# Optimization experiments

Hardware: AMD Instinct MI355X
Metric: run time of the kernel (lower is better)

Reference implementation:

```python
import math
import jax, jax.numpy as jnp
import numpy as np

N, CH3, T = 64, 192, 2048

def setup_inputs() -> dict:
    key = jax.random.key(0)
    qkv = jax.random.normal(key, (N, CH3, T), dtype=jnp.float32)
    return {"qkv": qkv}

def reference(qkv):
    ch = qkv.shape[1] // 3
    q, k, v = jnp.split(qkv, 3, axis=1)  # each [b, c, t]
    scale = 1.0 / math.sqrt(math.sqrt(ch))
    # [b, t, s] score matrix (faithful to the naive implementation)
    weight = jnp.einsum('bct,bcs->bts', q * scale, k * scale)
    weight = jax.nn.softmax(weight.astype(jnp.float32), axis=-1).astype(weight.dtype)
    return jnp.einsum('bts,bcs->bct', weight, v)
```

## Files before the change

kernel.cpp:

```cpp
#include <hip/hip_runtime.h>
#include <math.h>


#define B_     64
#define CH_    64
#define T_     2048
#define TQ     128
#define SB     64
#define NIT    (T_ / SB)
#define TILE_E 4096

typedef __attribute__((ext_vector_type(8))) short short8;
typedef __attribute__((ext_vector_type(4))) float f32x4;
typedef __attribute__((ext_vector_type(16))) float f32x16;
typedef __attribute__((ext_vector_type(4))) unsigned short us4;
typedef __attribute__((ext_vector_type(8))) unsigned short us8;

static __device__ __forceinline__ unsigned short f2bf(float f) {
    union { float f; unsigned u; } v; v.f = f;
    unsigned r = v.u + 0x7FFFu + ((v.u >> 16) & 1u);
    return (unsigned short)(r >> 16);
}

static __device__ __forceinline__ short8 ld_contig(const unsigned short* p) {
    return *(const short8*)p;
}

static __device__ __forceinline__ short8 ld_strided(const unsigned short* p, int stride) {
    short8 r;
#pragma unroll
    for (int j = 0; j < 8; ++j) r[j] = (short)p[j * stride];
    return r;
}

static __device__ __forceinline__ void gl_lds16(const unsigned short* g, unsigned short* l) {
    __builtin_amdgcn_global_load_lds(
        (const __attribute__((address_space(1))) unsigned int*)g,
        (__attribute__((address_space(3))) unsigned int*)l, 16, 0, 0);
}

static __device__ __forceinline__ float vexp2(float x) {
#if __has_builtin(__builtin_amdgcn_exp2f)
    return __builtin_amdgcn_exp2f(x);
#else
    float r;
    asm("v_exp_f32 %0, %1\n\ts_nop 1" : "=v"(r) : "v"(x));
    return r;
#endif
}

static __device__ __forceinline__ unsigned cvtpk(float lo, float hi) {
    unsigned r;
    asm("v_cvt_pk_bf16_f32 %0, %1, %2" : "=v"(r) : "v"(lo), "v"(hi));
    return r;
}

static __device__ __forceinline__ void pl32(unsigned& a, unsigned& b) {
    asm("v_permlane32_swap_b32 %0, %1" : "+v"(a), "+v"(b));
}

static __device__ __forceinline__ void pl_swap(unsigned& a, unsigned& b) {
    asm("v_permlane32_swap_b32 %0, %1" : "+v"(a), "+v"(b));
    asm("v_permlane16_swap_b32 %0, %1" : "+v"(a), "+v"(b));
}

__global__ __launch_bounds__(256) void qkv_prep(const float* __restrict__ qkv,
                                                unsigned short* __restrict__ Ktg,
                                                unsigned short* __restrict__ Vbg)
{
    __shared__ float Tl[64][65];
    const int tid = threadIdx.x;
    const int b   = blockIdx.x >> 5;
    const int st  = blockIdx.x & 31;
    const int s0  = st * 64;
    const float* Kp = qkv + (size_t)b * (3 * CH_ * T_) + (size_t)CH_ * T_;
    const float* Vp = Kp + (size_t)CH_ * T_;
    const size_t tbase = (size_t)(b * 32 + st) * TILE_E;

    {
        const int c = tid & 63, fq = tid >> 6;
#pragma unroll
        for (int k = 0; k < 4; ++k) {
            const int tl = 16 * fq + 4 * k;
            const float4 v = *(const float4*)(Kp + (size_t)c * T_ + s0 + tl);
            Tl[c][tl] = v.x; Tl[c][tl + 1] = v.y; Tl[c][tl + 2] = v.z; Tl[c][tl + 3] = v.w;
        }
    }

    {
        const int R = tid >> 2;
        const int m = tid & 3;
        const float* vin = Vp + (size_t)R * T_ + s0 + 16 * m;
        const float4 a0 = *(const float4*)(vin);
        const float4 a1 = *(const float4*)(vin + 4);
        const float4 a2 = *(const float4*)(vin + 8);
        const float4 a3 = *(const float4*)(vin + 12);
        us8 w0, w1;
        w0[0]=f2bf(a0.x); w0[1]=f2bf(a0.y); w0[2]=f2bf(a0.z); w0[3]=f2bf(a0.w);
        w0[4]=f2bf(a1.x); w0[5]=f2bf(a1.y); w0[6]=f2bf(a1.z); w0[7]=f2bf(a1.w);
        w1[0]=f2bf(a2.x); w1[1]=f2bf(a2.y); w1[2]=f2bf(a2.z); w1[3]=f2bf(a2.w);
        w1[4]=f2bf(a3.x); w1[5]=f2bf(a3.y); w1[6]=f2bf(a3.z); w1[7]=f2bf(a3.w);
        const int o = ((R >> 5) << 8) + (m << 6) + (R & 31);
        *(us8*)(Vbg + tbase + (size_t)o * 8)        = w0;
        *(us8*)(Vbg + tbase + (size_t)(o + 32) * 8) = w1;
    }
    __syncthreads();

    {
#pragma unroll
        for (int j2 = 0; j2 < 2; ++j2) {
            const int o = j2 * 256 + tid;
            const int R = j2 * 32 + (tid & 31);
            const int g = 2 * (tid >> 6) + ((tid >> 5) & 1);
            us8 w8;
#pragma unroll
            for (int j = 0; j < 8; ++j) w8[j] = f2bf(Tl[8 * g + j][R]);
            *(us8*)(Ktg + tbase + (size_t)o * 8) = w8;
        }
    }
}

__global__ __launch_bounds__(256, 4) void qkv_attn14(const float* __restrict__ qkv,
                                                     const unsigned short* __restrict__ Ktg,
                                                     const unsigned short* __restrict__ Vbg,
                                                     float* __restrict__ out)
{
    __shared__ unsigned short Ks[2][TILE_E];
    __shared__ unsigned short Vs[2][TILE_E];

    const int tid  = threadIdx.x;
    const int lane = tid & 63;
    const int wid  = tid >> 6;
    const int l31  = lane & 31;
    const int hi   = lane >> 5;

    int bid = blockIdx.x;
    bid = (bid & 7) * 128 + (bid >> 3);
    const int b  = bid >> 4;
    const int t0 = (bid & 15) * TQ;
    const int tb = t0 + wid * 32;

    const float* Qp = qkv + (size_t)b * (3 * CH_ * T_);
    const unsigned short* Ktb = Ktg + (size_t)b * 32 * TILE_E;
    const unsigned short* Vtb = Vbg + (size_t)b * 32 * TILE_E;

    const unsigned short* ksrc = Ktb + (size_t)tid * 8;
    const unsigned short* vsrc = Vtb + (size_t)tid * 8;
    const int lrd = lane * 8;

    short8 aq[4];
#pragma unroll
    for (int ks = 0; ks < 4; ++ks) {
        short8 q;
#pragma unroll
        for (int j = 0; j < 8; ++j)
            q[j] = (short)f2bf(0.180336880f *
                    Qp[(size_t)(16 * ks + 8 * hi + j) * T_ + tb + l31]);
        aq[ks] = q;
    }

    f32x16 zero16;
#pragma unroll
    for (int r = 0; r < 16; ++r) zero16[r] = 0.0f;
    f32x16 o0 = zero16, o1 = zero16;
    float dsum = 0.0f;

    gl_lds16(ksrc,        &Ks[0][wid * 512]);
    gl_lds16(ksrc + 2048, &Ks[0][2048 + wid * 512]);
    gl_lds16(vsrc,        &Vs[0][wid * 512]);
    gl_lds16(vsrc + 2048, &Vs[0][2048 + wid * 512]);

    for (int it = 0; it < NIT; ++it) {
        __syncthreads();
        const int buf = it & 1;
        if (it + 1 < NIT) {
            const unsigned short* kn = ksrc + (size_t)(it + 1) * TILE_E;
            const unsigned short* vn = vsrc + (size_t)(it + 1) * TILE_E;
            const int bo = (buf ^ 1) * TILE_E;
            gl_lds16(kn,        &Ks[0][bo + wid * 512]);
            gl_lds16(kn + 2048, &Ks[0][bo + 2048 + wid * 512]);
            gl_lds16(vn,        &Vs[0][bo + wid * 512]);
            gl_lds16(vn + 2048, &Vs[0][bo + 2048 + wid * 512]);
        }
        const unsigned short* kb = &Ks[buf][0];
        const unsigned short* vb = &Vs[buf][0];

        __builtin_amdgcn_s_setprio(1);

        f32x16 w0 = zero16, w1 = zero16;
#pragma unroll
        for (int ks = 0; ks < 4; ++ks) {
            const short8 k0 = ld_contig(kb + ks * 512 + lrd);
            const short8 k1 = ld_contig(kb + 2048 + ks * 512 + lrd);
            w0 = __builtin_amdgcn_mfma_f32_32x32x16_bf16(k0, aq[ks], w0, 0, 0, 0);
            w1 = __builtin_amdgcn_mfma_f32_32x32x16_bf16(k1, aq[ks], w1, 0, 0, 0);
        }

#pragma unroll
        for (int st = 0; st < 2; ++st) {
            float e[16];
#pragma unroll
            for (int r = 0; r < 16; ++r) e[r] = vexp2(st ? w1[r] : w0[r]);
            dsum += (((e[0] + e[1]) + (e[2] + e[3])) + ((e[4] + e[5]) + (e[6] + e[7])))
                  + (((e[8] + e[9]) + (e[10] + e[11])) + ((e[12] + e[13]) + (e[14] + e[15])));
            unsigned P0 = cvtpk(e[0], e[1]);
            unsigned P1 = cvtpk(e[2], e[3]);
            unsigned P2 = cvtpk(e[4], e[5]);
            unsigned P3 = cvtpk(e[6], e[7]);
            unsigned P4 = cvtpk(e[8], e[9]);
            unsigned P5 = cvtpk(e[10], e[11]);
            unsigned P6 = cvtpk(e[12], e[13]);
            unsigned P7 = cvtpk(e[14], e[15]);
            pl32(P0, P2);
            pl32(P1, P3);
            pl32(P4, P6);
            pl32(P5, P7);
            union { short8 s8; unsigned u[4]; } pba, pbb;
            pba.u[0] = P0; pba.u[1] = P1; pba.u[2] = P2; pba.u[3] = P3;
            pbb.u[0] = P4; pbb.u[1] = P5; pbb.u[2] = P6; pbb.u[3] = P7;
            const short8 va0 = ld_contig(vb + (2 * st) * 512 + lrd);
            const short8 va1 = ld_contig(vb + (2 * st + 1) * 512 + lrd);
            const short8 vb0 = ld_contig(vb + 2048 + (2 * st) * 512 + lrd);
            const short8 vb1 = ld_contig(vb + 2048 + (2 * st + 1) * 512 + lrd);
            o0 = __builtin_amdgcn_mfma_f32_32x32x16_bf16(va0, pba.s8, o0, 0, 0, 0);
            o0 = __builtin_amdgcn_mfma_f32_32x32x16_bf16(va1, pbb.s8, o0, 0, 0, 0);
            o1 = __builtin_amdgcn_mfma_f32_32x32x16_bf16(vb0, pba.s8, o1, 0, 0, 0);
            o1 = __builtin_amdgcn_mfma_f32_32x32x16_bf16(vb1, pbb.s8, o1, 0, 0, 0);
        }
        __builtin_amdgcn_s_setprio(0);
    }

    float d = dsum + __shfl_xor(dsum, 32, 64);
    const float inv = 1.0f / d;

    float* outp = out + (size_t)b * CH_ * T_;
#pragma unroll
    for (int r = 0; r < 16; ++r) {
        const int crow = (r & 3) + 8 * (r >> 2) + 4 * hi;
        outp[(size_t)crow * T_ + tb + l31]        = o0[r] * inv;
        outp[(size_t)(32 + crow) * T_ + tb + l31] = o1[r] * inv;
    }
}

__global__ __launch_bounds__(256) void qkv_attn_fb(const float* __restrict__ qkv,
                                                   float* __restrict__ out)
{
    __shared__ unsigned short Qs[CH_][68];
    __shared__ unsigned short Ksf[CH_][68];
    __shared__ unsigned short Vsf[CH_][72];
    __shared__ unsigned short Psf[4][64][18];

    const int tid  = threadIdx.x;
    const int lane = tid & 63;
    const int wid  = tid >> 6;
    const int l15  = lane & 15;
    const int h    = lane >> 4;
    const int bidx = blockIdx.x;
    const int b    = bidx >> 5;
    const int t0   = (bidx & 31) * 64;
    const int tw   = wid * 16;

    const float* Qp = qkv + (size_t)b * (3 * CH_ * T_);
    const float* Kp = Qp + CH_ * T_;
    const float* Vp = Kp + CH_ * T_;

    const int srow = tid >> 4;
    const int scol = (tid & 15) << 2;

#pragma unroll
    for (int i = 0; i < 4; ++i) {
        const int c = srow + 16 * i;
        const float4 q = *(const float4*)(Qp + (size_t)c * T_ + t0 + scol);
        us4 w; w[0] = f2bf(q.x); w[1] = f2bf(q.y); w[2] = f2bf(q.z); w[3] = f2bf(q.w);
        *(us4*)(&Qs[c][scol]) = w;
    }
    __syncthreads();

    const short8 aq0 = ld_strided(&Qs[0 + 8 * h][tw + l15], 68);
    const short8 aq1 = ld_strided(&Qs[32 + 8 * h][tw + l15], 68);

    short8 aones;
#pragma unroll
    for (int j = 0; j < 8; ++j) aones[j] = (short)0x3F80;

    f32x4 o[4];
#pragma unroll
    for (int cs = 0; cs < 4; ++cs) o[cs] = (f32x4){0.f, 0.f, 0.f, 0.f};
    float l_run = 0.0f;
    const f32x4 zero4 = {0.f, 0.f, 0.f, 0.f};

    for (int it = 0; it < 32; ++it) {
        const int s0 = it * 64;
        __syncthreads();
#pragma unroll
        for (int i = 0; i < 4; ++i) {
            const int c = srow + 16 * i;
            const float4 kv = *(const float4*)(Kp + (size_t)c * T_ + s0 + scol);
            us4 wk; wk[0] = f2bf(kv.x); wk[1] = f2bf(kv.y); wk[2] = f2bf(kv.z); wk[3] = f2bf(kv.w);
            *(us4*)(&Ksf[c][scol]) = wk;
            const float4 vv = *(const float4*)(Vp + (size_t)c * T_ + s0 + scol);
            us4 wv; wv[0] = f2bf(vv.x); wv[1] = f2bf(vv.y); wv[2] = f2bf(vv.z); wv[3] = f2bf(vv.w);
            *(us4*)(&Vsf[c][scol]) = wv;
        }
        __syncthreads();

        f32x4 w[4];
#pragma unroll
        for (int ss = 0; ss < 4; ++ss) {
            const short8 bkl = ld_strided(&Ksf[0 + 8 * h][ss * 16 + l15], 68);
            const short8 bkh = ld_strided(&Ksf[32 + 8 * h][ss * 16 + l15], 68);
            f32x4 acc = zero4;
            acc = __builtin_amdgcn_mfma_f32_16x16x32_bf16(aq0, bkl, acc, 0, 0, 0);
            acc = __builtin_amdgcn_mfma_f32_16x16x32_bf16(aq1, bkh, acc, 0, 0, 0);
            w[ss] = acc;
        }

#pragma unroll
        for (int ss = 0; ss < 4; ++ss) {
            const float e0 = __expf(0.125f * w[ss][0]);
            const float e1 = __expf(0.125f * w[ss][1]);
            const float e2 = __expf(0.125f * w[ss][2]);
            const float e3 = __expf(0.125f * w[ss][3]);
            const unsigned p01 = (unsigned)f2bf(e0) | ((unsigned)f2bf(e1) << 16);
            const unsigned p23 = (unsigned)f2bf(e2) | ((unsigned)f2bf(e3) << 16);
            const int s = ss * 16 + l15;
            *(unsigned*)(&Psf[wid][s][4 * h]) = p01;
            *(unsigned*)(&Psf[wid][s][4 * h + 2]) = p23;
        }

        const short8 pb0 = ld_strided(&Psf[wid][0 + 8 * h][l15], 18);
        const short8 pb1 = ld_strided(&Psf[wid][32 + 8 * h][l15], 18);

        f32x4 lacc = zero4;
        lacc = __builtin_amdgcn_mfma_f32_16x16x32_bf16(aones, pb0, lacc, 0, 0, 0);
        lacc = __builtin_amdgcn_mfma_f32_16x16x32_bf16(aones, pb1, lacc, 0, 0, 0);
        l_run += lacc[0];

#pragma unroll
        for (int cs = 0; cs < 4; ++cs) {
            us4 lo0 = *(const us4*)(&Vsf[cs * 16 + l15][0 + 8 * h]);
            us4 hi0 = *(const us4*)(&Vsf[cs * 16 + l15][4 + 8 * h]);
            us4 lo1 = *(const us4*)(&Vsf[cs * 16 + l15][32 + 8 * h]);
            us4 hi1 = *(const us4*)(&Vsf[cs * 16 + l15][36 + 8 * h]);
            short8 av0, av1;
            av0[0]=(short)lo0[0]; av0[1]=(short)lo0[1]; av0[2]=(short)lo0[2]; av0[3]=(short)lo0[3];
            av0[4]=(short)hi0[0]; av0[5]=(short)hi0[1]; av0[6]=(short)hi0[2]; av0[7]=(short)hi0[3];
            av1[0]=(short)lo1[0]; av1[1]=(short)lo1[1]; av1[2]=(short)lo1[2]; av1[3]=(short)lo1[3];
            av1[4]=(short)hi1[0]; av1[5]=(short)hi1[1]; av1[6]=(short)hi1[2]; av1[7]=(short)hi1[3];
            o[cs] = __builtin_amdgcn_mfma_f32_16x16x32_bf16(av0, pb0, o[cs], 0, 0, 0);
            o[cs] = __builtin_amdgcn_mfma_f32_16x16x32_bf16(av1, pb1, o[cs], 0, 0, 0);
        }
    }

    const float invd = 1.0f / l_run;
    float* outp = out + (size_t)b * CH_ * T_;
#pragma unroll
    for (int cs = 0; cs < 4; ++cs)
#pragma unroll
        for (int r = 0; r < 4; ++r)
            outp[(size_t)(cs * 16 + 4 * h + r) * T_ + t0 + tw + l15] = o[cs][r] * invd;
}

extern "C" void kernel_launch(void* const* d_in, const int* in_sizes, int n_in,
                              void* d_out, int out_size, void* d_ws, size_t ws_size,
                              hipStream_t stream) {
    const float* qkv = (const float*)d_in[0];
    float* outp = (float*)d_out;
    const size_t need = (size_t)2 * B_ * CH_ * T_ * sizeof(unsigned short);
    if (ws_size >= need) {
        unsigned short* Ktg = (unsigned short*)d_ws;
        unsigned short* Vbg = Ktg + (size_t)B_ * T_ * CH_;
        qkv_prep<<<dim3(B_ * 32), dim3(256), 0, stream>>>(qkv, Ktg, Vbg);
        qkv_attn14<<<dim3(B_ * (T_ / TQ)), dim3(256), 0, stream>>>(qkv, Ktg, Vbg, outp);
    } else {
        qkv_attn_fb<<<dim3(B_ * 32), dim3(256), 0, stream>>>(qkv, outp);
    }
}
```

Before: 94.48 us.

## Software-pipeline QK scores one tile ahead with triple-buffered V in LDS

Measured after the change: 94.93 us. Within noise of the previous version (+0.5%).

```diff
diff --git a/kernel.cpp b/kernel.cpp
--- a/kernel.cpp
+++ b/kernel.cpp
@@ -120,13 +120,13 @@
     }
 }
 
-__global__ __launch_bounds__(256, 4) void qkv_attn14(const float* __restrict__ qkv,
+__global__ __launch_bounds__(256, 4) void qkv_attn15(const float* __restrict__ qkv,
                                                      const unsigned short* __restrict__ Ktg,
                                                      const unsigned short* __restrict__ Vbg,
                                                      float* __restrict__ out)
 {
     __shared__ unsigned short Ks[2][TILE_E];
-    __shared__ unsigned short Vs[2][TILE_E];
+    __shared__ unsigned short Vs3[3 * TILE_E];
 
     const int tid  = threadIdx.x;
     const int lane = tid & 63;
@@ -147,6 +147,7 @@
     const unsigned short* ksrc = Ktb + (size_t)tid * 8;
     const unsigned short* vsrc = Vtb + (size_t)tid * 8;
     const int lrd = lane * 8;
+    const int sofs = wid * 512;
 
     short8 aq[4];
 #pragma unroll
@@ -165,42 +166,61 @@
     f32x16 o0 = zero16, o1 = zero16;
     float dsum = 0.0f;
 
-    gl_lds16(ksrc,        &Ks[0][wid * 512]);
-    gl_lds16(ksrc + 2048, &Ks[0][2048 + wid * 512]);
-    gl_lds16(vsrc,        &Vs[0][wid * 512]);
-    gl_lds16(vsrc + 2048, &Vs[0][2048 + wid * 512]);
-
-    for (int it = 0; it < NIT; ++it) {
+    gl_lds16(ksrc,        &Ks[0][sofs]);
+    gl_lds16(ksrc + 2048, &Ks[0][2048 + sofs]);
+    gl_lds16(vsrc,        &Vs3[sofs]);
+    gl_lds16(vsrc + 2048, &Vs3[2048 + sofs]);
+
+    f32x16 wc0, wc1;
+    {
         __syncthreads();
-        const int buf = it & 1;
+        gl_lds16(ksrc + TILE_E,        &Ks[1][sofs]);
+        gl_lds16(ksrc + TILE_E + 2048, &Ks[1][2048 + sofs]);
+        gl_lds16(vsrc + TILE_E,        &Vs3[TILE_E + sofs]);
+        gl_lds16(vsrc + TILE_E + 2048, &Vs3[TILE_E + 2048 + sofs]);
+        const unsigned short* kb = &Ks[0][0];
+        f32x16 a = zero16, c = zero16;
+#pragma unroll
+        for (int ks = 0; ks < 4; ++ks) {
+            const short8 k0 = ld_contig(kb + ks * 512 + lrd);
+            const short8 k1 = ld_contig(kb + 2048 + ks * 512 + lrd);
+            a = __builtin_amdgcn_mfma_f32_32x32x16_bf16(k0, aq[ks], a, 0, 0, 0);
+            c = __builtin_amdgcn_mfma_f32_32x32x16_bf16(k1, aq[ks], c, 0, 0, 0);
+        }
+        wc0 = a; wc1 = c;
+    }
+
+    int vr = 0, vw = 2;
+    for (int it = 1; it < NIT; ++it) {
+        __syncthreads();
+        const int kbuf = it & 1;
         if (it + 1 < NIT) {
             const unsigned short* kn = ksrc + (size_t)(it + 1) * TILE_E;
             const unsigned short* vn = vsrc + (size_t)(it + 1) * TILE_E;
-            const int bo = (buf ^ 1) * TILE_E;
-            gl_lds16(kn,        &Ks[0][bo + wid * 512]);
-            gl_lds16(kn + 2048, &Ks[0][bo + 2048 + wid * 512]);
-            gl_lds16(vn,        &Vs[0][bo + wid * 512]);
-            gl_lds16(vn + 2048, &Vs[0][bo + 2048 + wid * 512]);
-        }
-        const unsigned short* kb = &Ks[buf][0];
-        const unsigned short* vb = &Vs[buf][0];
+            gl_lds16(kn,        &Ks[kbuf ^ 1][sofs]);
+            gl_lds16(kn + 2048, &Ks[kbuf ^ 1][2048 + sofs]);
+            gl_lds16(vn,        &Vs3[vw * TILE_E + sofs]);
+            gl_lds16(vn + 2048, &Vs3[vw * TILE_E + 2048 + sofs]);
+        }
 
         __builtin_amdgcn_s_setprio(1);
 
-        f32x16 w0 = zero16, w1 = zero16;
+        const unsigned short* kb = &Ks[kbuf][0];
+        f32x16 wn0 = zero16, wn1 = zero16;
 #pragma unroll
         for (int ks = 0; ks < 4; ++ks) {
             const short8 k0 = ld_contig(kb + ks * 512 + lrd);
             const short8 k1 = ld_contig(kb + 2048 + ks * 512 + lrd);
-            w0 = __builtin_amdgcn_mfma_f32_32x32x16_bf16(k0, aq[ks], w0, 0, 0, 0);
-            w1 = __builtin_amdgcn_mfma_f32_32x32x16_bf16(k1, aq[ks], w1, 0, 0, 0);
-        }
-
+            wn0 = __builtin_amdgcn_mfma_f32_32x32x16_bf16(k0, aq[ks], wn0, 0, 0, 0);
+            wn1 = __builtin_amdgcn_mfma_f32_32x32x16_bf16(k1, aq[ks], wn1, 0, 0, 0);
+        }
+
+        const unsigned short* vb = &Vs3[vr * TILE_E];
 #pragma unroll
         for (int st = 0; st < 2; ++st) {
             float e[16];
 #pragma unroll
-            for (int r = 0; r < 16; ++r) e[r] = vexp2(st ? w1[r] : w0[r]);
+            for (int r = 0; r < 16; ++r) e[r] = vexp2(st ? wc1[r] : wc0[r]);
             dsum += (((e[0] + e[1]) + (e[2] + e[3])) + ((e[4] + e[5]) + (e[6] + e[7])))
                   + (((e[8] + e[9]) + (e[10] + e[11])) + ((e[12] + e[13]) + (e[14] + e[15])));
             unsigned P0 = cvtpk(e[0], e[1]);
@@ -228,6 +248,45 @@
             o1 = __builtin_amdgcn_mfma_f32_32x32x16_bf16(vb1, pbb.s8, o1, 0, 0, 0);
         }
         __builtin_amdgcn_s_setprio(0);
+
+        wc0 = wn0; wc1 = wn1;
+        vr = (vr + 1 < 3) ? vr + 1 : 0;
+        vw = (vw + 1 < 3) ? vw + 1 : 0;
+    }
+
+    {
+        const unsigned short* vb = &Vs3[vr * TILE_E];
+#pragma unroll
+        for (int st = 0; st < 2; ++st) {
+            float e[16];
+#pragma unroll
+            for (int r = 0; r < 16; ++r) e[r] = vexp2(st ? wc1[r] : wc0[r]);
+            dsum += (((e[0] + e[1]) + (e[2] + e[3])) + ((e[4] + e[5]) + (e[6] + e[7])))
+                  + (((e[8] + e[9]) + (e[10] + e[11])) + ((e[12] + e[13]) + (e[14] + e[15])));
+            unsigned P0 = cvtpk(e[0], e[1]);
+            unsigned P1 = cvtpk(e[2], e[3]);
+            unsigned P2 = cvtpk(e[4], e[5]);
+            unsigned P3 = cvtpk(e[6], e[7]);
+            unsigned P4 = cvtpk(e[8], e[9]);
+            unsigned P5 = cvtpk(e[10], e[11]);
+            unsigned P6 = cvtpk(e[12], e[13]);
+            unsigned P7 = cvtpk(e[14], e[15]);
+            pl32(P0, P2);
+            pl32(P1, P3);
+            pl32(P4, P6);
+            pl32(P5, P7);
+            union { short8 s8; unsigned u[4]; } pba, pbb;
+            pba.u[0] = P0; pba.u[1] = P1; pba.u[2] = P2; pba.u[3] = P3;
+            pbb.u[0] = P4; pbb.u[1] = P5; pbb.u[2] = P6; pbb.u[3] = P7;
+            const short8 va0 = ld_contig(vb + (2 * st) * 512 + lrd);
+            const short8 va1 = ld_contig(vb + (2 * st + 1) * 512 + lrd);
+            const short8 vb0 = ld_contig(vb + 2048 + (2 * st) * 512 + lrd);
+            const short8 vb1 = ld_contig(vb + 2048 + (2 * st + 1) * 512 + lrd);
+            o0 = __builtin_amdgcn_mfma_f32_32x32x16_bf16(va0, pba.s8, o0, 0, 0, 0);
+            o0 = __builtin_amdgcn_mfma_f32_32x32x16_bf16(va1, pbb.s8, o0, 0, 0, 0);
+            o1 = __builtin_amdgcn_mfma_f32_32x32x16_bf16(vb0, pba.s8, o1, 0, 0, 0);
+            o1 = __builtin_amdgcn_mfma_f32_32x32x16_bf16(vb1, pbb.s8, o1, 0, 0, 0);
+        }
     }
 
     float d = dsum + __shfl_xor(dsum, 32, 64);
@@ -371,7 +430,7 @@
         unsigned short* Ktg = (unsigned short*)d_ws;
         unsigned short* Vbg = Ktg + (size_t)B_ * T_ * CH_;
         qkv_prep<<<dim3(B_ * 32), dim3(256), 0, stream>>>(qkv, Ktg, Vbg);
-        qkv_attn14<<<dim3(B_ * (T_ / TQ)), dim3(256), 0, stream>>>(qkv, Ktg, Vbg, outp);
+        qkv_attn15<<<dim3(B_ * (T_ / TQ)), dim3(256), 0, stream>>>(qkv, Ktg, Vbg, outp);
     } else {
         qkv_attn_fb<<<dim3(B_ * 32), dim3(256), 0, stream>>>(qkv, outp);
     }
```

## Process two query sub-tiles per wave to reuse K/V fragments

Applied to the files above, without the earlier changes.

Result: no change. 93.52 us (-1.0%).

```diff
diff --git a/kernel.cpp b/kernel.cpp
--- a/kernel.cpp
+++ b/kernel.cpp
@@ -5,7 +5,7 @@
 #define B_     64
 #define CH_    64
 #define T_     2048
-#define TQ     128
+#define TQ     256
 #define SB     64
 #define NIT    (T_ / SB)
 #define TILE_E 4096
@@ -44,24 +44,49 @@
     return __builtin_amdgcn_exp2f(x);
 #else
     float r;
-    asm("v_exp_f32 %0, %1\n\ts_nop 1" : "=v"(r) : "v"(x));
+    asm volatile("v_exp_f32 %0, %1\n\ts_nop 1" : "=v"(r) : "v"(x));
     return r;
 #endif
 }
 
 static __device__ __forceinline__ unsigned cvtpk(float lo, float hi) {
     unsigned r;
-    asm("v_cvt_pk_bf16_f32 %0, %1, %2" : "=v"(r) : "v"(lo), "v"(hi));
+    asm volatile("v_cvt_pk_bf16_f32 %0, %1, %2" : "=v"(r) : "v"(lo), "v"(hi));
     return r;
 }
 
 static __device__ __forceinline__ void pl32(unsigned& a, unsigned& b) {
-    asm("v_permlane32_swap_b32 %0, %1" : "+v"(a), "+v"(b));
+    asm volatile("v_permlane32_swap_b32 %0, %1" : "+v"(a), "+v"(b));
 }
 
 static __device__ __forceinline__ void pl_swap(unsigned& a, unsigned& b) {
-    asm("v_permlane32_swap_b32 %0, %1" : "+v"(a), "+v"(b));
-    asm("v_permlane16_swap_b32 %0, %1" : "+v"(a), "+v"(b));
+    asm volatile("v_permlane32_swap_b32 %0, %1" : "+v"(a), "+v"(b));
+    asm volatile("v_permlane16_swap_b32 %0, %1" : "+v"(a), "+v"(b));
+}
+
+static __device__ __forceinline__ void softmax_pack(const f32x16& w, float& dsum,
+                                                    short8& pba, short8& pbb) {
+    float e[16];
+#pragma unroll
+    for (int r = 0; r < 16; ++r) e[r] = vexp2(w[r]);
+    dsum += (((e[0] + e[1]) + (e[2] + e[3])) + ((e[4] + e[5]) + (e[6] + e[7])))
+          + (((e[8] + e[9]) + (e[10] + e[11])) + ((e[12] + e[13]) + (e[14] + e[15])));
+    unsigned P0 = cvtpk(e[0], e[1]);
+    unsigned P1 = cvtpk(e[2], e[3]);
+    unsigned P2 = cvtpk(e[4], e[5]);
+    unsigned P3 = cvtpk(e[6], e[7]);
+    unsigned P4 = cvtpk(e[8], e[9]);
+    unsigned P5 = cvtpk(e[10], e[11]);
+    unsigned P6 = cvtpk(e[12], e[13]);
+    unsigned P7 = cvtpk(e[14], e[15]);
+    pl32(P0, P2);
+    pl32(P1, P3);
+    pl32(P4, P6);
+    pl32(P5, P7);
+    union { short8 s8; unsigned u[4]; } a, b;
+    a.u[0] = P0; a.u[1] = P1; a.u[2] = P2; a.u[3] = P3;
+    b.u[0] = P4; b.u[1] = P5; b.u[2] = P6; b.u[3] = P7;
+    pba = a.s8; pbb = b.s8;
 }
 
 __global__ __launch_bounds__(256) void qkv_prep(const float* __restrict__ qkv,
@@ -120,7 +145,7 @@
     }
 }
 
-__global__ __launch_bounds__(256, 4) void qkv_attn14(const float* __restrict__ qkv,
+__global__ __launch_bounds__(256, 2) void qkv_attn17(const float* __restrict__ qkv,
                                                      const unsigned short* __restrict__ Ktg,
                                                      const unsigned short* __restrict__ Vbg,
                                                      float* __restrict__ out)
@@ -135,10 +160,10 @@
     const int hi   = lane >> 5;
 
     int bid = blockIdx.x;
-    bid = (bid & 7) * 128 + (bid >> 3);
-    const int b  = bid >> 4;
-    const int t0 = (bid & 15) * TQ;
-    const int tb = t0 + wid * 32;
+    bid = (bid & 7) * 64 + (bid >> 3);
+    const int b  = bid >> 3;
+    const int t0 = (bid & 7) * TQ;
+    const int tb = t0 + wid * 64;
 
     const float* Qp = qkv + (size_t)b * (3 * CH_ * T_);
     const unsigned short* Ktb = Ktg + (size_t)b * 32 * TILE_E;
@@ -147,28 +172,31 @@
     const unsigned short* ksrc = Ktb + (size_t)tid * 8;
     const unsigned short* vsrc = Vtb + (size_t)tid * 8;
     const int lrd = lane * 8;
-
-    short8 aq[4];
+    const int sofs = wid * 512;
+
+    short8 aq0[4], aq1[4];
 #pragma unroll
     for (int ks = 0; ks < 4; ++ks) {
-        short8 q;
-#pragma unroll
-        for (int j = 0; j < 8; ++j)
-            q[j] = (short)f2bf(0.180336880f *
-                    Qp[(size_t)(16 * ks + 8 * hi + j) * T_ + tb + l31]);
-        aq[ks] = q;
+        short8 q0, q1;
+#pragma unroll
+        for (int j = 0; j < 8; ++j) {
+            const float* qrow = Qp + (size_t)(16 * ks + 8 * hi + j) * T_ + tb + l31;
+            q0[j] = (short)f2bf(0.180336880f * qrow[0]);
+            q1[j] = (short)f2bf(0.180336880f * qrow[32]);
+        }
+        aq0[ks] = q0; aq1[ks] = q1;
     }
 
     f32x16 zero16;
 #pragma unroll
     for (int r = 0; r < 16; ++r) zero16[r] = 0.0f;
-    f32x16 o0 = zero16, o1 = zero16;
-    float dsum = 0.0f;
-
-    gl_lds16(ksrc,        &Ks[0][wid * 512]);
-    gl_lds16(ksrc + 2048, &Ks[0][2048 + wid * 512]);
-    gl_lds16(vsrc,        &Vs[0][wid * 512]);
-    gl_lds16(vsrc + 2048, &Vs[0][2048 + wid * 512]);
+    f32x16 o00 = zero16, o01 = zero16, o10 = zero16, o11 = zero16;
+    float dsum0 = 0.0f, dsum1 = 0.0f;
+
+    gl_lds16(ksrc,        &Ks[0][sofs]);
+    gl_lds16(ksrc + 2048, &Ks[0][2048 + sofs]);
+    gl_lds16(vsrc,        &Vs[0][sofs]);
+    gl_lds16(vsrc + 2048, &Vs[0][2048 + sofs]);
 
     for (int it = 0; it < NIT; ++it) {
         __syncthreads();
@@ -177,68 +205,64 @@
             const unsigned short* kn = ksrc + (size_t)(it + 1) * TILE_E;
             const unsigned short* vn = vsrc + (size_t)(it + 1) * TILE_E;
             const int bo = (buf ^ 1) * TILE_E;
-            gl_lds16(kn,        &Ks[0][bo + wid * 512]);
-            gl_lds16(kn + 2048, &Ks[0][bo + 2048 + wid * 512]);
-            gl_lds16(vn,        &Vs[0][bo + wid * 512]);
-            gl_lds16(vn + 2048, &Vs[0][bo + 2048 + wid * 512]);
+            gl_lds16(kn,        &Ks[0][bo + sofs]);
+            gl_lds16(kn + 2048, &Ks[0][bo + 2048 + sofs]);
+            gl_lds16(vn,        &Vs[0][bo + sofs]);
+            gl_lds16(vn + 2048, &Vs[0][bo + 2048 + sofs]);
         }
         const unsigned short* kb = &Ks[buf][0];
         const unsigned short* vb = &Vs[buf][0];
 
         __builtin_amdgcn_s_setprio(1);
 
-        f32x16 w0 = zero16, w1 = zero16;
-#pragma unroll
-        for (int ks = 0; ks < 4; ++ks) {
-            const short8 k0 = ld_contig(kb + ks * 512 + lrd);
-            const short8 k1 = ld_contig(kb + 2048 + ks * 512 + lrd);
-            w0 = __builtin_amdgcn_mfma_f32_32x32x16_bf16(k0, aq[ks], w0, 0, 0, 0);
-            w1 = __builtin_amdgcn_mfma_f32_32x32x16_bf16(k1, aq[ks], w1, 0, 0, 0);
-        }
-
 #pragma unroll
         for (int st = 0; st < 2; ++st) {
-            float e[16];
-#pragma unroll
-            for (int r = 0; r < 16; ++r) e[r] = vexp2(st ? w1[r] : w0[r]);
-            dsum += (((e[0] + e[1]) + (e[2] + e[3])) + ((e[4] + e[5]) + (e[6] + e[7])))
-                  + (((e[8] + e[9]) + (e[10] + e[11])) + ((e[12] + e[13]) + (e[14] + e[15])));
-            unsigned P0 = cvtpk(e[0], e[1]);
-            unsigned P1 = cvtpk(e[2], e[3]);
-            unsigned P2 = cvtpk(e[4], e[5]);
-            unsigned P3 = cvtpk(e[6], e[7]);
-            unsigned P4 = cvtpk(e[8], e[9]);
-            unsigned P5 = cvtpk(e[10], e[11]);
-            unsigned P6 = cvtpk(e[12], e[13]);
-            unsigned P7 = cvtpk(e[14], e[15]);
-            pl32(P0, P2);
-            pl32(P1, P3);
-            pl32(P4, P6);
-            pl32(P5, P7);
-            union { short8 s8; unsigned u[4]; } pba, pbb;
-            pba.u[0] = P0; pba.u[1] = P1; pba.u[2] = P2; pba.u[3] = P3;
-            pbb.u[0] = P4; pbb.u[1] = P5; pbb.u[2] = P6; pbb.u[3] = P7;
-            const short8 va0 = ld_contig(vb + (2 * st) * 512 + lrd);
-            const short8 va1 = ld_contig(vb + (2 * st + 1) * 512 + lrd);
-            const short8 vb0 = ld_contig(vb + 2048 + (2 * st) * 512 + lrd);
-            const short8 vb1 = ld_contig(vb + 2048 + (2 * st + 1) * 512 + lrd);
-            o0 = __builtin_amdgcn_mfma_f32_32x32x16_bf16(va0, pba.s8, o0, 0, 0, 0);
-            o0 = __builtin_amdgcn_mfma_f32_32x32x16_bf16(va1, pbb.s8, o0, 0, 0, 0);
-            o1 = __builtin_amdgcn_mfma_f32_32x32x16_bf16(vb0, pba.s8, o1, 0, 0, 0);
-            o1 = __builtin_amdgcn_mfma_f32_32x32x16_bf16(vb1, pbb.s8, o1, 0, 0, 0);
+            f32x16 wA = zero16, wB = zero16;
+#pragma unroll
+            for (int ks = 0; ks < 4; ++ks) {
+                const short8 k0 = ld_contig(kb + st * 2048 + ks * 512 + lrd);
+                wA = __builtin_amdgcn_mfma_f32_32x32x16_bf16(k0, aq0[ks], wA, 0, 0, 0);
+                wB = __builtin_amdgcn_mfma_f32_32x32x16_bf16(k0, aq1[ks], wB, 0, 0, 0);
+            }
+
+            const short8 v00 = ld_contig(vb + (2 * st) * 512 + lrd);
+            const short8 v01 = ld_contig(vb + (2 * st + 1) * 512 + lrd);
+            const short8 v10 = ld_contig(vb + 2048 + (2 * st) * 512 + lrd);
+            const short8 v11 = ld_contig(vb + 2048 + (2 * st + 1) * 512 + lrd);
+
+            {
+                short8 pba, pbb;
+                softmax_pack(wA, dsum0, pba, pbb);
+                o00 = __builtin_amdgcn_mfma_f32_32x32x16_bf16(v00, pba, o00, 0, 0, 0);
+                o00 = __builtin_amdgcn_mfma_f32_32x32x16_bf16(v01, pbb, o00, 0, 0, 0);
+                o10 = __builtin_amdgcn_mfma_f32_32x32x16_bf16(v10, pba, o10, 0, 0, 0);
+                o10 = __builtin_amdgcn_mfma_f32_32x32x16_bf16(v11, pbb, o10, 0, 0, 0);
+            }
+            {
+                short8 pba, pbb;
+                softmax_pack(wB, dsum1, pba, pbb);
+                o01 = __builtin_amdgcn_mfma_f32_32x32x16_bf16(v00, pba, o01, 0, 0, 0);
+                o01 = __builtin_amdgcn_mfma_f32_32x32x16_bf16(v01, pbb, o01, 0, 0, 0);
+                o11 = __builtin_amdgcn_mfma_f32_32x32x16_bf16(v10, pba, o11, 0, 0, 0);
+                o11 = __builtin_amdgcn_mfma_f32_32x32x16_bf16(v11, pbb, o11, 0, 0, 0);
+            }
         }
         __builtin_amdgcn_s_setprio(0);
     }
 
-    float d = dsum + __shfl_xor(dsum, 32, 64);
-    const float inv = 1.0f / d;
+    const float inv0 = 1.0f / (dsum0 + __shfl_xor(dsum0, 32, 64));
+    const float inv1 = 1.0f / (dsum1 + __shfl_xor(dsum1, 32, 64));
 
     float* outp = out + (size_t)b * CH_ * T_;
 #pragma unroll
     for (int r = 0; r < 16; ++r) {
         const int crow = (r & 3) + 8 * (r >> 2) + 4 * hi;
-        outp[(size_t)crow * T_ + tb + l31]        = o0[r] * inv;
-        outp[(size_t)(32 + crow) * T_ + tb + l31] = o1[r] * inv;
+        float* row0 = outp + (size_t)crow * T_ + tb + l31;
+        float* row1 = outp + (size_t)(32 + crow) * T_ + tb + l31;
+        row0[0]  = o00[r] * inv0;
+        row0[32] = o01[r] * inv1;
+        row1[0]  = o10[r] * inv0;
+        row1[32] = o11[r] * inv1;
     }
 }
 
@@ -371,7 +395,7 @@
         unsigned short* Ktg = (unsigned short*)d_ws;
         unsigned short* Vbg = Ktg + (size_t)B_ * T_ * CH_;
         qkv_prep<<<dim3(B_ * 32), dim3(256), 0, stream>>>(qkv, Ktg, Vbg);
-        qkv_attn14<<<dim3(B_ * (T_ / TQ)), dim3(256), 0, stream>>>(qkv, Ktg, Vbg, outp);
+        qkv_attn17<<<dim3(B_ * (T_ / TQ)), dim3(256), 0, stream>>>(qkv, Ktg, Vbg, outp);
     } else {
         qkv_attn_fb<<<dim3(B_ * 32), dim3(256), 0, stream>>>(qkv, outp);
     }
```
